# Performance work log

Hardware: AMD Instinct MI355X
Metric: run time of the kernel (lower is better)

Reference implementation:

```python
import jax, jax.numpy as jnp
import numpy as np

ALPHA = 0.2  # LeakyReLU negative slope
NEG = -9e15


def _gat_heads(x, adj_mask, W, a):
    # x: (B,N,F); W: (H,F,O); a: (H,2O); adj_mask: (B,N,N) bool
    O = W.shape[-1]
    Wh = jnp.einsum('bnf,hfo->bhno', x, W)            # (B,H,N,O)
    e1 = jnp.einsum('bhno,ho->bhn', Wh, a[:, :O])     # Wh @ a[:O]
    e2 = jnp.einsum('bhno,ho->bhn', Wh, a[:, O:])     # Wh @ a[O:]
    e = jax.nn.leaky_relu(e1[:, :, :, None] + e2[:, :, None, :], ALPHA)  # (B,H,N,N)
    e = jnp.where(adj_mask[:, None], e, NEG)
    attn = jax.nn.softmax(e, axis=-1)
    return jnp.einsum('bhnm,bhmo->bhno', attn, Wh)    # (B,H,N,O)


def _gat_block(x, adj_mask, non_pad_mask, W_heads, a_heads, W_out, a_out):
    # multi-head layer, concat=True -> elu per head, then concat on feature dim
    h = jax.nn.elu(_gat_heads(x, adj_mask, W_heads, a_heads))  # (B,H,N,O)
    B, H, N, O = h.shape
    h = jnp.transpose(h, (0, 2, 1, 3)).reshape(B, N, H * O)
    h = h * non_pad_mask
    # out layer: single head, concat=False (no inner elu)
    h = _gat_heads(h, adj_mask, W_out[None], a_out[None])[:, 0]  # (B,N,noutput)
    h = h * non_pad_mask
    return jax.nn.elu(h)


def setup_inputs() -> dict:
    key = jax.random.key(0)
    ks = jax.random.split(key, 8)
    B, N = 32, 256
    vocab, F, O, H, OUT = 200, 300, 256, 8, 512
    fea = jax.random.randint(ks[0], (B, N), 0, vocab, dtype=jnp.int32)
    adj = jax.random.randint(ks[1], (B, N, N), 0, 2, dtype=jnp.int32)
    non_pad_mask = jnp.ones((B, N, 1), dtype=jnp.float32)
    embed = jax.random.normal(ks[2], (vocab, F), dtype=jnp.float32)
    W_heads = jax.random.normal(ks[3], (H, F, O), dtype=jnp.float32) / np.sqrt(F)
    a_heads = jax.random.normal(ks[4], (H, 2 * O), dtype=jnp.float32) / np.sqrt(2 * O)
    W_out = jax.random.normal(ks[5], (H * O, OUT), dtype=jnp.float32) / np.sqrt(H * O)
    a_out = jax.random.normal(ks[6], (2 * OUT,), dtype=jnp.float32) / np.sqrt(2 * OUT)
    return {"fea": fea, "adj": adj, "non_pad_mask": non_pad_mask, "embed": embed,
            "W_heads": W_heads, "a_heads": a_heads, "W_out": W_out, "a_out": a_out}


def reference(fea, adj, non_pad_mask, embed, W_heads, a_heads, W_out, a_out):
    adj_mask = adj > 0
    x = embed[fea]  # (B,N,F)
    # GAT_num = 1; dropout is identity in eval mode
    x = _gat_block(x, adj_mask, non_pad_mask, W_heads, a_heads, W_out, a_out)
    return x  # (B, N, 512)
```

## Files before the change

### kernel.cpp

```cpp
#include <hip/hip_runtime.h>
#include <math.h>


typedef _Float16 f16;
typedef __attribute__((ext_vector_type(8))) _Float16 f16x8;
typedef __attribute__((ext_vector_type(4))) _Float16 f16x4;
typedef __attribute__((ext_vector_type(4))) float f32x4;
typedef unsigned long long u64;

__device__ __forceinline__ void async16(const void* g, void* lds) {
  __builtin_amdgcn_global_load_lds(
      (const __attribute__((address_space(1))) void*)g,
      (__attribute__((address_space(3))) void*)lds, 16, 0, 0);
}

__global__ __launch_bounds__(256) void k_prep(const int* __restrict__ fea,
                                              const float* __restrict__ embed,
                                              const float* __restrict__ Whd,
                                              const float* __restrict__ Wo,
                                              const int* __restrict__ adj,
                                              const float* __restrict__ ah,
                                              f16* __restrict__ x16,
                                              f16* __restrict__ WcT,
                                              f16* __restrict__ WoT,
                                              float* __restrict__ e_all,
                                              u64* __restrict__ adjG,
                                              float* __restrict__ w12G) {
  int bid = blockIdx.x, tid = threadIdx.x;
  if (bid < 1280) {
    int idx = bid * 256 + tid;
    int row = idx / 40, c = idx % 40;
    int tok = fea[row];
    const float* eb = embed + (size_t)tok * 300;
    f16x8 v;
    if (c < 37) {
      float4 f0 = *(const float4*)&eb[c * 8];
      float4 f1 = *(const float4*)&eb[c * 8 + 4];
      v[0] = (f16)f0.x; v[1] = (f16)f0.y; v[2] = (f16)f0.z; v[3] = (f16)f0.w;
      v[4] = (f16)f1.x; v[5] = (f16)f1.y; v[6] = (f16)f1.z; v[7] = (f16)f1.w;
    } else {
#pragma unroll
      for (int j = 0; j < 8; ++j) {
        int t = c * 8 + j;
        v[j] = (f16)((t < 300) ? eb[t] : 0.f);
      }
    }
    *(f16x8*)&x16[(size_t)row * 320 + c * 8] = v;
  } else if (bid < 1920) {
    int r = bid - 1280;
    int zi = r * 256 + tid;
    if (zi < 16384) e_all[zi] = 0.f;
    __shared__ float tile[32][33];
    int bx = r % 10, q0 = r / 10;
    int by = q0 % 8, h = q0 / 8;
    int c = tid & 31, q = tid >> 5;
#pragma unroll
    for (int i = 0; i < 4; ++i) {
      int tt = q + i * 8;
      int t = bx * 32 + tt;
      float v = (t < 300) ? Whd[((size_t)h * 300 + t) * 256 + by * 32 + c] : 0.f;
      tile[tt][c] = v;
    }
    __syncthreads();
#pragma unroll
    for (int i = 0; i < 4; ++i) {
      int oo = q + i * 8;
      int gc = h * 256 + by * 32 + oo;
      WcT[(size_t)gc * 320 + bx * 32 + c] = (f16)tile[c][oo];
    }
  } else if (bid < 2944) {
    int r = bid - 1920;
    __shared__ float tile[32][33];
    int bx = r % 64, by = r / 64;
    int c = tid & 31, q = tid >> 5;
#pragma unroll
    for (int i = 0; i < 4; ++i) {
      int kk = q + i * 8;
      tile[kk][c] = Wo[((size_t)bx * 32 + kk) * 512 + by * 32 + c];
    }
    __syncthreads();
#pragma unroll
    for (int i = 0; i < 4; ++i) {
      int oo = q + i * 8;
      WoT[((size_t)by * 32 + oo) * 2048 + bx * 32 + c] = (f16)tile[c][oo];
    }
  } else if (bid < 3072) {
    int r = bid - 2944;
    int wv = tid >> 6, ln = tid & 63;
    int row = r * 64 + wv * 16;
    const int* ar = adj + (size_t)row * 256;
#pragma unroll 4
    for (int i = 0; i < 16; ++i, ar += 256) {
      u64 m0 = __ballot(ar[ln] != 0);
      u64 m1 = __ballot(ar[64 + ln] != 0);
      u64 m2 = __ballot(ar[128 + ln] != 0);
      u64 m3 = __ballot(ar[192 + ln] != 0);
      if (ln == 0) {
        u64* d = &adjG[(size_t)(row + i) * 4];
        d[0] = m0; d[1] = m1; d[2] = m2; d[3] = m3;
      }
    }
  } else {
    int hh = bid - 3072;
    __shared__ float a1s[256], a2s[256];
    a1s[tid] = ah[hh * 512 + tid];
    a2s[tid] = ah[hh * 512 + 256 + tid];
    __syncthreads();
    for (int t = tid; t < 320; t += 256) {
      float s1 = 0.f, s2 = 0.f;
      if (t < 300) {
        const float* wr = Whd + ((size_t)hh * 300 + t) * 256;
#pragma unroll 4
        for (int o = 0; o < 256; o += 4) {
          float4 w4 = *(const float4*)&wr[o];
          s1 += w4.x * a1s[o] + w4.y * a1s[o + 1] + w4.z * a1s[o + 2] + w4.w * a1s[o + 3];
          s2 += w4.x * a2s[o] + w4.y * a2s[o + 1] + w4.z * a2s[o + 2] + w4.w * a2s[o + 3];
        }
      }
      w12G[hh * 640 + t] = s1;
      w12G[hh * 640 + 320 + t] = s2;
    }
  }
}

__global__ __launch_bounds__(256, 2) void k_l1(
    const f16* __restrict__ x16, const f16* __restrict__ WcT,
    const float* __restrict__ w12G, const u64* __restrict__ adjG,
    const float* __restrict__ npm, f16* __restrict__ h1) {
  extern __shared__ __align__(16) char smem[];
  f16* As = (f16*)smem;
  f16* Bs = (f16*)(smem + 32768);
  char* WhB = smem;
  u64* adjB = (u64*)(smem + 65536);
  float* e2f = (float*)(smem + 73728);
  float* e1f = (float*)(smem + 74752);
  float* wl  = (float*)(smem + 75776);

  const int bid = blockIdx.x;
  const int xcd = bid & 7, inner = bid >> 3;
  const int oh = inner & 1;
  const int h = (inner >> 1) & 7;
  const int b = (inner >> 4) * 8 + xcd;
  const int tid = threadIdx.x;
  const int wave = tid >> 6, lane = tid & 63;
  const int lrow = lane & 15, quad = lane >> 4;
  const int srow = lane >> 3;
  const int scol = ((lane & 7) ^ (lane >> 3)) * 8;
  const int l7 = lrow & 7;

  async16((const char*)adjG + (size_t)b * 8192 + tid * 16, (char*)adjB + tid * 16);
  async16((const char*)adjG + (size_t)b * 8192 + 4096 + tid * 16,
          (char*)adjB + 4096 + tid * 16);
  if (tid < 160) async16((const char*)w12G + h * 2560 + tid * 16, (char*)wl + tid * 16);
  __syncthreads();

  {
    const f16* xrow = x16 + ((size_t)b * 256 + tid) * 320;
    float e1 = 0.f, e2 = 0.f;
#pragma unroll 8
    for (int c = 0; c < 40; ++c) {
      f16x8 xv = *(const f16x8*)&xrow[c * 8];
#pragma unroll
      for (int j = 0; j < 8; ++j) {
        float xf = (float)xv[j];
        e1 += xf * wl[c * 8 + j];
        e2 += xf * wl[320 + c * 8 + j];
      }
    }
    e1f[tid] = e1;
    e2f[tid] = e2;
  }

  f32x4 acc[4][8] = {};
  const f16* Ag = x16 + (size_t)b * 256 * 320;
  const f16* Bg = WcT + ((size_t)(h * 256 + oh * 128)) * 320;

  for (int t = 0; t < 5; ++t) {
    const int k0 = t * 64;
    __syncthreads();
#pragma unroll
    for (int j = 0; j < 8; ++j) {
      const int r0 = wave * 64 + j * 8;
      async16(Ag + (size_t)(r0 + srow) * 320 + k0 + scol, &As[r0 * 64]);
    }
#pragma unroll
    for (int j = 0; j < 4; ++j) {
      const int r0 = wave * 32 + j * 8;
      async16(Bg + (size_t)(r0 + srow) * 320 + k0 + scol, &Bs[r0 * 64]);
    }
    __syncthreads();
#pragma unroll
    for (int s = 0; s < 2; ++s) {
      const int sq = ((s * 4 + quad) ^ l7) * 8;
      f16x8 af[4], bf[8];
#pragma unroll
      for (int mt = 0; mt < 4; ++mt)
        af[mt] = *(const f16x8*)&As[(wave * 64 + mt * 16 + lrow) * 64 + sq];
#pragma unroll
      for (int nt = 0; nt < 8; ++nt)
        bf[nt] = *(const f16x8*)&Bs[(nt * 16 + lrow) * 64 + sq];
#pragma unroll
      for (int mt = 0; mt < 4; ++mt)
#pragma unroll
        for (int nt = 0; nt < 8; ++nt)
          acc[mt][nt] = __builtin_amdgcn_mfma_f32_16x16x32_f16(af[mt], bf[nt], acc[mt][nt], 0, 0, 0);
    }
  }
  __syncthreads();

#pragma unroll
  for (int mt = 0; mt < 4; ++mt) {
    const int n0 = wave * 64 + mt * 16 + quad * 4;
    const int q16 = n0 >> 3;
    const int hoff = (n0 & 4) ? 8 : 0;
#pragma unroll
    for (int nt = 0; nt < 8; ++nt) {
      const int o = nt * 16 + lrow;
      f16x4 v;
#pragma unroll
      for (int r = 0; r < 4; ++r) v[r] = (f16)acc[mt][nt][r];
      *(f16x4*)(WhB + o * 512 + ((q16 ^ (o & 7)) * 16 + hoff)) = v;
    }
  }
  __syncthreads();

  float4 e2q = *(const float4*)&e2f[lane * 4];
  float e2m = fmaxf(fmaxf(e2q.x, e2q.y), fmaxf(e2q.z, e2q.w));
#pragma unroll
  for (int m = 1; m < 64; m <<= 1) e2m = fmaxf(e2m, __shfl_xor(e2m, m));

  float er[4], sh[4];
  u64 aw[4][4];
#pragma unroll
  for (int g = 0; g < 4; ++g) {
    int n = wave * 64 + g * 16 + lrow;
    er[g] = e1f[n];
    float s = er[g] + e2m;
    sh[g] = s > 0.f ? s : 0.2f * s;
#pragma unroll
    for (int q = 0; q < 4; ++q) aw[g][q] = adjB[n * 4 + q];
  }

  f16x8 P[4][8];
  float ss[4] = {0.f, 0.f, 0.f, 0.f};
#pragma unroll
  for (int k0 = 0; k0 < 8; ++k0) {
    const float* e2p = &e2f[k0 * 32 + quad * 8];
    float4 ea = *(const float4*)e2p;
    float4 eb = *(const float4*)(e2p + 4);
    float e2arr[8] = {ea.x, ea.y, ea.z, ea.w, eb.x, eb.y, eb.z, eb.w};
#pragma unroll
    for (int g = 0; g < 4; ++g) {
      unsigned int bits = (unsigned int)(aw[g][k0 >> 1] >> ((k0 & 1) * 32 + quad * 8)) & 0xFFu;
      f16x8 q;
#pragma unroll
      for (int j = 0; j < 8; ++j) {
        float v = er[g] + e2arr[j];
        v = v > 0.f ? v : 0.2f * v;
        float p = (bits >> j) & 1 ? __expf(v - sh[g]) : 0.f;
        ss[g] += p;
        q[j] = (f16)p;
      }
      P[g][k0] = q;
    }
  }
  float rs[4], pm[4];
  f16* hb[4];
#pragma unroll
  for (int g = 0; g < 4; ++g) {
    ss[g] += __shfl_xor(ss[g], 16);
    ss[g] += __shfl_xor(ss[g], 32);
    rs[g] = 1.f / ss[g];
    int n = wave * 64 + g * 16 + lrow;
    pm[g] = npm[b * 256 + n];
    hb[g] = &h1[((size_t)(b * 256 + n)) * 2048 + h * 256 + oh * 128];
  }

#pragma unroll 2
  for (int of = 0; of < 8; ++of) {
    const int ol = of * 16 + lrow;
    const char* wo = WhB + ol * 512;
    f32x4 c[4] = {};
#pragma unroll
    for (int k0 = 0; k0 < 8; ++k0) {
      f16x8 af = *(const f16x8*)(wo + (((k0 * 4 + quad) ^ (ol & 7)) * 16));
#pragma unroll
      for (int g = 0; g < 4; ++g)
        c[g] = __builtin_amdgcn_mfma_f32_16x16x32_f16(af, P[g][k0], c[g], 0, 0, 0);
    }
    const int o0 = of * 16 + quad * 4;
#pragma unroll
    for (int g = 0; g < 4; ++g) {
      f16x4 st;
#pragma unroll
      for (int r = 0; r < 4; ++r) {
        float v = c[g][r] * rs[g];
        v = v > 0.f ? v : (__expf(v) - 1.f);
        st[r] = (f16)(v * pm[g]);
      }
      *(f16x4*)(hb[g] + o0) = st;
    }
  }
}

__global__ __launch_bounds__(256, 4) void k_gemm_sk(const f16* __restrict__ A,
                                                    const f16* __restrict__ BT,
                                                    f16* __restrict__ outSK,
                                                    const float* __restrict__ ao,
                                                    float* __restrict__ e12,
                                                    float* __restrict__ e22) {
  __shared__ f16 As[128 * 64];
  __shared__ f16 Bs[64 * 64];
  const int bid = blockIdx.x;
  const int xcd = bid & 7, j5 = bid >> 3;
  const int bx = j5 & 7;
  const int kz = (j5 >> 6) & 1;
  const int by = xcd * 8 + ((j5 >> 3) & 7);
  const int tid = threadIdx.x;
  const int wave = tid >> 6, lane = tid & 63;
  const int wm = wave >> 1, wn = wave & 1;
  const int lrow = lane & 15, quad = lane >> 4;
  const int srow = lane >> 3;
  const int scol = ((lane & 7) ^ (lane >> 3)) * 8;
  const int l7 = lrow & 7;

  f32x4 acc[4][2] = {};
  const f16* Ag = A + (size_t)by * 128 * 2048;
  const f16* Bg = BT + (size_t)bx * 64 * 2048;
  const int kbeg = kz * 1024;

  for (int k0 = kbeg; k0 < kbeg + 1024; k0 += 64) {
    __syncthreads();
#pragma unroll
    for (int j = 0; j < 4; ++j) {
      const int r0 = wave * 32 + j * 8;
      async16(Ag + (size_t)(r0 + srow) * 2048 + k0 + scol, &As[r0 * 64]);
    }
#pragma unroll
    for (int j = 0; j < 2; ++j) {
      const int r0 = wave * 16 + j * 8;
      async16(Bg + (size_t)(r0 + srow) * 2048 + k0 + scol, &Bs[r0 * 64]);
    }
    __syncthreads();
#pragma unroll
    for (int s = 0; s < 2; ++s) {
      const int sq = ((s * 4 + quad) ^ l7) * 8;
      f16x8 af[4], bf[2];
#pragma unroll
      for (int t = 0; t < 4; ++t)
        af[t] = *(const f16x8*)&As[(wm * 64 + t * 16 + lrow) * 64 + sq];
#pragma unroll
      for (int t = 0; t < 2; ++t)
        bf[t] = *(const f16x8*)&Bs[(wn * 32 + t * 16 + lrow) * 64 + sq];
#pragma unroll
      for (int mt = 0; mt < 4; ++mt)
#pragma unroll
        for (int nt = 0; nt < 2; ++nt)
          acc[mt][nt] = __builtin_amdgcn_mfma_f32_16x16x32_f16(af[mt], bf[nt], acc[mt][nt], 0, 0, 0);
    }
  }

  const int b = (by * 128) >> 8;
  const int nbase0 = (by * 128) & 255;
  f16* dst = outSK + (size_t)kz * 32 * 512 * 256;
#pragma unroll
  for (int mt = 0; mt < 4; ++mt) {
    const int nb = nbase0 + wm * 64 + mt * 16 + quad * 4;
#pragma unroll
    for (int nt = 0; nt < 2; ++nt) {
      const int gc = bx * 64 + wn * 32 + nt * 16 + lrow;
      f16x4 v;
#pragma unroll
      for (int r = 0; r < 4; ++r) v[r] = (f16)acc[mt][nt][r];
      *(f16x4*)&dst[((size_t)b * 512 + gc) * 256 + nb] = v;
    }
  }

  float a1v[2], a2v[2];
#pragma unroll
  for (int nt = 0; nt < 2; ++nt) {
    const int gc = bx * 64 + wn * 32 + nt * 16 + lrow;
    a1v[nt] = ao[gc];
    a2v[nt] = ao[512 + gc];
  }
#pragma unroll
  for (int mt = 0; mt < 4; ++mt) {
    float s1[4] = {0.f, 0.f, 0.f, 0.f}, s2[4] = {0.f, 0.f, 0.f, 0.f};
#pragma unroll
    for (int nt = 0; nt < 2; ++nt)
#pragma unroll
      for (int r = 0; r < 4; ++r) {
        s1[r] += acc[mt][nt][r] * a1v[nt];
        s2[r] += acc[mt][nt][r] * a2v[nt];
      }
#pragma unroll
    for (int r = 0; r < 4; ++r)
#pragma unroll
      for (int m = 1; m < 16; m <<= 1) {
        s1[r] += __shfl_xor(s1[r], m);
        s2[r] += __shfl_xor(s2[r], m);
      }
    if (lrow == 0) {
      const int nb = nbase0 + wm * 64 + mt * 16 + quad * 4;
#pragma unroll
      for (int r = 0; r < 4; ++r) {
        atomicAdd(&e12[b * 256 + nb + r], s1[r]);
        atomicAdd(&e22[b * 256 + nb + r], s2[r]);
      }
    }
  }
}

#define PSTRIDE 264

__global__ __launch_bounds__(256, 4) void k_attn2(
    const f16* __restrict__ sk, const float* __restrict__ e1g, const float* __restrict__ e2g,
    const u64* __restrict__ adjG, const float* __restrict__ npm, float* __restrict__ out) {
  int bid = blockIdx.x;
  int nt0 = (bid >> 3) & 3;
  int pair = (bid >> 5) * 8 + (bid & 7);
  int oh = pair >> 5, b = pair & 31;
  int n0 = nt0 * 64;
  __shared__ f16 P[64 * PSTRIDE];
  int tid = threadIdx.x;
  int wave = tid >> 6, lane = tid & 63;
  int lrow = lane & 15, quad = lane >> 4;

  const f16* Ag0 = sk + ((size_t)b * 512 + oh * 128) * 256;
  const f16* Ag1 = Ag0 + (size_t)32 * 512 * 256;
  f16x8 afp0[2], afp1[2];
#pragma unroll
  for (int mt = 0; mt < 2; ++mt) {
    size_t off = (size_t)(wave * 32 + mt * 16 + lrow) * 256 + quad * 8;
    afp0[mt] = *(const f16x8*)&Ag0[off];
    afp1[mt] = *(const f16x8*)&Ag1[off];
  }

  float4 e2v = *(const float4*)&e2g[b * 256 + lane * 4];
  float e2m = fmaxf(fmaxf(e2v.x, e2v.y), fmaxf(e2v.z, e2v.w));
#pragma unroll
  for (int m = 1; m < 64; m <<= 1) e2m = fmaxf(e2m, __shfl_xor(e2m, m));
#pragma unroll 4
  for (int i = 0; i < 16; ++i) {
    int row = i * 4 + wave;
    int gn = b * 256 + n0 + row;
    float er = e1g[b * 256 + n0 + row];
    float sh = er + e2m;
    sh = sh > 0.f ? sh : 0.2f * sh;
    u64 word = adjG[(size_t)gn * 4 + (lane >> 4)];
    unsigned int bits = (unsigned int)(word >> ((lane & 15) * 4)) & 0xFu;
    float p0, p1, p2, p3;
    {
      float v = er + e2v.x; v = v > 0.f ? v : 0.2f * v;
      p0 = bits & 1 ? __expf(v - sh) : 0.f;
      v = er + e2v.y; v = v > 0.f ? v : 0.2f * v;
      p1 = bits & 2 ? __expf(v - sh) : 0.f;
      v = er + e2v.z; v = v > 0.f ? v : 0.2f * v;
      p2 = bits & 4 ? __expf(v - sh) : 0.f;
      v = er + e2v.w; v = v > 0.f ? v : 0.2f * v;
      p3 = bits & 8 ? __expf(v - sh) : 0.f;
    }
    float sm = p0 + p1 + p2 + p3;
#pragma unroll
    for (int m = 1; m < 64; m <<= 1) sm += __shfl_xor(sm, m);
    float rs = 1.f / sm;
    f16x4 pw;
    pw[0] = (f16)(p0 * rs); pw[1] = (f16)(p1 * rs);
    pw[2] = (f16)(p2 * rs); pw[3] = (f16)(p3 * rs);
    *(f16x4*)&P[row * PSTRIDE + lane * 4] = pw;
  }
  __syncthreads();

  f32x4 acc[2][4] = {};
#pragma unroll
  for (int kk = 0; kk < 8; ++kk) {
    const int k0 = kk * 32;
    f16x8 af[2], bf[4];
#pragma unroll
    for (int mt = 0; mt < 2; ++mt) {
      if (kk == 0) {
        af[mt] = afp0[mt] + afp1[mt];
      } else {
        size_t off = (size_t)(wave * 32 + mt * 16 + lrow) * 256 + k0 + quad * 8;
        af[mt] = *(const f16x8*)&Ag0[off] + *(const f16x8*)&Ag1[off];
      }
    }
#pragma unroll
    for (int nt = 0; nt < 4; ++nt)
      bf[nt] = *(const f16x8*)&P[(nt * 16 + lrow) * PSTRIDE + k0 + quad * 8];
#pragma unroll
    for (int mt = 0; mt < 2; ++mt)
#pragma unroll
      for (int nt = 0; nt < 4; ++nt)
        acc[mt][nt] = __builtin_amdgcn_mfma_f32_16x16x32_f16(af[mt], bf[nt], acc[mt][nt], 0, 0, 0);
  }
#pragma unroll
  for (int nt = 0; nt < 4; ++nt) {
    int nloc = nt * 16 + lrow;
    int gn = b * 256 + n0 + nloc;
    float pm = npm[gn];
#pragma unroll
    for (int mt = 0; mt < 2; ++mt) {
      int o0 = oh * 128 + wave * 32 + mt * 16 + quad * 4;
      float4 st;
      float v0 = acc[mt][nt][0] * pm;
      float v1 = acc[mt][nt][1] * pm;
      float v2 = acc[mt][nt][2] * pm;
      float v3 = acc[mt][nt][3] * pm;
      st.x = v0 > 0.f ? v0 : (__expf(v0) - 1.f);
      st.y = v1 > 0.f ? v1 : (__expf(v1) - 1.f);
      st.z = v2 > 0.f ? v2 : (__expf(v2) - 1.f);
      st.w = v3 > 0.f ? v3 : (__expf(v3) - 1.f);
      *(float4*)&out[(size_t)gn * 512 + o0] = st;
    }
  }
}

extern "C" void kernel_launch(void* const* d_in, const int* in_sizes, int n_in,
                              void* d_out, int out_size, void* d_ws, size_t ws_size,
                              hipStream_t stream) {
  (void)in_sizes; (void)n_in; (void)out_size; (void)ws_size;
  const int*   fea   = (const int*)d_in[0];
  const int*   adj   = (const int*)d_in[1];
  const float* npm   = (const float*)d_in[2];
  const float* embed = (const float*)d_in[3];
  const float* Whd   = (const float*)d_in[4];
  const float* ah    = (const float*)d_in[5];
  const float* Wo    = (const float*)d_in[6];
  const float* ao    = (const float*)d_in[7];
  float* out = (float*)d_out;

  char* ws = (char*)d_ws;
  f16* x16  = (f16*)ws;  ws += (size_t)8192 * 320 * 2;
  f16* WcT  = (f16*)ws;  ws += (size_t)2048 * 320 * 2;
  f16* WoT  = (f16*)ws;  ws += (size_t)512 * 2048 * 2;
  f16* h1   = (f16*)ws;  ws += (size_t)8192 * 2048 * 2;
  f16* Wh2sk = (f16*)ws; ws += (size_t)2 * 32 * 512 * 256 * 2;
  float* e12 = (float*)ws; ws += (size_t)8192 * 4;
  float* e22 = (float*)ws; ws += (size_t)8192 * 4;
  u64* adjG = (u64*)ws;  ws += (size_t)8192 * 4 * 8;
  float* w12G = (float*)ws; ws += (size_t)8 * 640 * 4;

  k_prep<<<3080, 256, 0, stream>>>(fea, embed, Whd, Wo, adj, ah, x16, WcT, WoT, e12, adjG, w12G);

  k_l1<<<512, 256, 78336, stream>>>(x16, WcT, w12G, adjG, npm, h1);

  k_gemm_sk<<<1024, 256, 0, stream>>>(h1, WoT, Wh2sk, ao, e12, e22);
  k_attn2<<<512, 256, 0, stream>>>(Wh2sk, e12, e22, adjG, npm, out);
}
```

Measured before the change: 199.1 us.

## Double k_l1 block to 512 threads and split work across eight waves

Doubles the threads per block of the first-layer GAT kernel from 256 to 512. The GEMM tile is split 4x2 across waves, so each wave holds a 64x64 accumulator instead of 64x128. The e1/e2 dot products are split between thread halves, and each wave handles 32 attention rows instead of 64. This lowers per-thread register pressure and adds wave-level parallelism to hide latency. In exchange it adds more waves contending for the same 78 KB LDS block, which still limits occupancy to about two blocks per CU.

```diff
diff --git a/kernel.cpp b/kernel.cpp
--- a/kernel.cpp
+++ b/kernel.cpp
@@ -123,7 +123,7 @@
   }
 }
 
-__global__ __launch_bounds__(256, 2) void k_l1(
+__global__ __launch_bounds__(512, 4) void k_l1(
     const f16* __restrict__ x16, const f16* __restrict__ WcT,
     const float* __restrict__ w12G, const u64* __restrict__ adjG,
     const float* __restrict__ npm, f16* __restrict__ h1) {
@@ -132,8 +132,8 @@
   f16* Bs = (f16*)(smem + 32768);
   char* WhB = smem;
   u64* adjB = (u64*)(smem + 65536);
-  float* e2f = (float*)(smem + 73728);
-  float* e1f = (float*)(smem + 74752);
+  float* e1f = (float*)(smem + 73728);
+  float* e2f = (float*)(smem + 74752);
   float* wl  = (float*)(smem + 75776);
 
   const int bid = blockIdx.x;
@@ -143,35 +143,32 @@
   const int b = (inner >> 4) * 8 + xcd;
   const int tid = threadIdx.x;
   const int wave = tid >> 6, lane = tid & 63;
+  const int wm = wave >> 1, wn = wave & 1;
   const int lrow = lane & 15, quad = lane >> 4;
   const int srow = lane >> 3;
   const int scol = ((lane & 7) ^ (lane >> 3)) * 8;
   const int l7 = lrow & 7;
 
   async16((const char*)adjG + (size_t)b * 8192 + tid * 16, (char*)adjB + tid * 16);
-  async16((const char*)adjG + (size_t)b * 8192 + 4096 + tid * 16,
-          (char*)adjB + 4096 + tid * 16);
   if (tid < 160) async16((const char*)w12G + h * 2560 + tid * 16, (char*)wl + tid * 16);
   __syncthreads();
 
   {
-    const f16* xrow = x16 + ((size_t)b * 256 + tid) * 320;
-    float e1 = 0.f, e2 = 0.f;
+    const int n = tid & 255;
+    const float* wv = (tid < 256) ? wl : (wl + 320);
+    const f16* xrow = x16 + ((size_t)b * 256 + n) * 320;
+    float e = 0.f;
 #pragma unroll 8
     for (int c = 0; c < 40; ++c) {
       f16x8 xv = *(const f16x8*)&xrow[c * 8];
 #pragma unroll
-      for (int j = 0; j < 8; ++j) {
-        float xf = (float)xv[j];
-        e1 += xf * wl[c * 8 + j];
-        e2 += xf * wl[320 + c * 8 + j];
-      }
-    }
-    e1f[tid] = e1;
-    e2f[tid] = e2;
-  }
-
-  f32x4 acc[4][8] = {};
+      for (int j = 0; j < 8; ++j) e += (float)xv[j] * wv[c * 8 + j];
+    }
+    if (tid < 256) e1f[n] = e;
+    else e2f[n] = e;
+  }
+
+  f32x4 acc[4][4] = {};
   const f16* Ag = x16 + (size_t)b * 256 * 320;
   const f16* Bg = WcT + ((size_t)(h * 256 + oh * 128)) * 320;
 
@@ -179,30 +176,30 @@
     const int k0 = t * 64;
     __syncthreads();
 #pragma unroll
-    for (int j = 0; j < 8; ++j) {
-      const int r0 = wave * 64 + j * 8;
-      async16(Ag + (size_t)(r0 + srow) * 320 + k0 + scol, &As[r0 * 64]);
-    }
-#pragma unroll
     for (int j = 0; j < 4; ++j) {
       const int r0 = wave * 32 + j * 8;
+      async16(Ag + (size_t)(r0 + srow) * 320 + k0 + scol, &As[r0 * 64]);
+    }
+#pragma unroll
+    for (int j = 0; j < 2; ++j) {
+      const int r0 = wave * 16 + j * 8;
       async16(Bg + (size_t)(r0 + srow) * 320 + k0 + scol, &Bs[r0 * 64]);
     }
     __syncthreads();
 #pragma unroll
     for (int s = 0; s < 2; ++s) {
       const int sq = ((s * 4 + quad) ^ l7) * 8;
-      f16x8 af[4], bf[8];
+      f16x8 af[4], bf[4];
 #pragma unroll
       for (int mt = 0; mt < 4; ++mt)
-        af[mt] = *(const f16x8*)&As[(wave * 64 + mt * 16 + lrow) * 64 + sq];
-#pragma unroll
-      for (int nt = 0; nt < 8; ++nt)
-        bf[nt] = *(const f16x8*)&Bs[(nt * 16 + lrow) * 64 + sq];
+        af[mt] = *(const f16x8*)&As[(wm * 64 + mt * 16 + lrow) * 64 + sq];
+#pragma unroll
+      for (int nt = 0; nt < 4; ++nt)
+        bf[nt] = *(const f16x8*)&Bs[(wn * 64 + nt * 16 + lrow) * 64 + sq];
 #pragma unroll
       for (int mt = 0; mt < 4; ++mt)
 #pragma unroll
-        for (int nt = 0; nt < 8; ++nt)
+        for (int nt = 0; nt < 4; ++nt)
           acc[mt][nt] = __builtin_amdgcn_mfma_f32_16x16x32_f16(af[mt], bf[nt], acc[mt][nt], 0, 0, 0);
     }
   }
@@ -210,12 +207,12 @@
 
 #pragma unroll
   for (int mt = 0; mt < 4; ++mt) {
-    const int n0 = wave * 64 + mt * 16 + quad * 4;
+    const int n0 = wm * 64 + mt * 16 + quad * 4;
     const int q16 = n0 >> 3;
     const int hoff = (n0 & 4) ? 8 : 0;
 #pragma unroll
-    for (int nt = 0; nt < 8; ++nt) {
-      const int o = nt * 16 + lrow;
+    for (int nt = 0; nt < 4; ++nt) {
+      const int o = wn * 64 + nt * 16 + lrow;
       f16x4 v;
 #pragma unroll
       for (int r = 0; r < 4; ++r) v[r] = (f16)acc[mt][nt][r];
@@ -229,77 +226,72 @@
 #pragma unroll
   for (int m = 1; m < 64; m <<= 1) e2m = fmaxf(e2m, __shfl_xor(e2m, m));
 
-  float er[4], sh[4];
-  u64 aw[4][4];
-#pragma unroll
-  for (int g = 0; g < 4; ++g) {
-    int n = wave * 64 + g * 16 + lrow;
-    er[g] = e1f[n];
-    float s = er[g] + e2m;
-    sh[g] = s > 0.f ? s : 0.2f * s;
-#pragma unroll
-    for (int q = 0; q < 4; ++q) aw[g][q] = adjB[n * 4 + q];
-  }
-
-  f16x8 P[4][8];
-  float ss[4] = {0.f, 0.f, 0.f, 0.f};
+  const int nb0 = wave * 32;
+  const float er0 = e1f[nb0 + lrow];
+  const float er1 = e1f[nb0 + 16 + lrow];
+  float sh0 = er0 + e2m; sh0 = sh0 > 0.f ? sh0 : 0.2f * sh0;
+  float sh1 = er1 + e2m; sh1 = sh1 > 0.f ? sh1 : 0.2f * sh1;
+  u64 aw0[4], aw1[4];
+#pragma unroll
+  for (int q = 0; q < 4; ++q) {
+    aw0[q] = adjB[(nb0 + lrow) * 4 + q];
+    aw1[q] = adjB[(nb0 + 16 + lrow) * 4 + q];
+  }
+
+  f16x8 p0[8], p1[8];
+  float ss0 = 0.f, ss1 = 0.f;
 #pragma unroll
   for (int k0 = 0; k0 < 8; ++k0) {
     const float* e2p = &e2f[k0 * 32 + quad * 8];
     float4 ea = *(const float4*)e2p;
     float4 eb = *(const float4*)(e2p + 4);
+    unsigned int b0 = (unsigned int)(aw0[k0 >> 1] >> ((k0 & 1) * 32 + quad * 8)) & 0xFFu;
+    unsigned int b1 = (unsigned int)(aw1[k0 >> 1] >> ((k0 & 1) * 32 + quad * 8)) & 0xFFu;
     float e2arr[8] = {ea.x, ea.y, ea.z, ea.w, eb.x, eb.y, eb.z, eb.w};
-#pragma unroll
-    for (int g = 0; g < 4; ++g) {
-      unsigned int bits = (unsigned int)(aw[g][k0 >> 1] >> ((k0 & 1) * 32 + quad * 8)) & 0xFFu;
-      f16x8 q;
-#pragma unroll
-      for (int j = 0; j < 8; ++j) {
-        float v = er[g] + e2arr[j];
-        v = v > 0.f ? v : 0.2f * v;
-        float p = (bits >> j) & 1 ? __expf(v - sh[g]) : 0.f;
-        ss[g] += p;
-        q[j] = (f16)p;
-      }
-      P[g][k0] = q;
-    }
-  }
-  float rs[4], pm[4];
-  f16* hb[4];
-#pragma unroll
-  for (int g = 0; g < 4; ++g) {
-    ss[g] += __shfl_xor(ss[g], 16);
-    ss[g] += __shfl_xor(ss[g], 32);
-    rs[g] = 1.f / ss[g];
-    int n = wave * 64 + g * 16 + lrow;
-    pm[g] = npm[b * 256 + n];
-    hb[g] = &h1[((size_t)(b * 256 + n)) * 2048 + h * 256 + oh * 128];
-  }
+    f16x8 q0, q1;
+#pragma unroll
+    for (int j = 0; j < 8; ++j) {
+      float v = er0 + e2arr[j]; v = v > 0.f ? v : 0.2f * v;
+      float p = (b0 >> j) & 1 ? __expf(v - sh0) : 0.f;
+      ss0 += p; q0[j] = (f16)p;
+      v = er1 + e2arr[j]; v = v > 0.f ? v : 0.2f * v;
+      p = (b1 >> j) & 1 ? __expf(v - sh1) : 0.f;
+      ss1 += p; q1[j] = (f16)p;
+    }
+    p0[k0] = q0; p1[k0] = q1;
+  }
+  ss0 += __shfl_xor(ss0, 16); ss0 += __shfl_xor(ss0, 32);
+  ss1 += __shfl_xor(ss1, 16); ss1 += __shfl_xor(ss1, 32);
+  const float rs0 = 1.f / ss0, rs1 = 1.f / ss1;
+  const float pm0 = npm[b * 256 + nb0 + lrow];
+  const float pm1 = npm[b * 256 + nb0 + 16 + lrow];
+  f16* h1b0 = &h1[(size_t)(b * 256 + nb0 + lrow) * 2048 + h * 256 + oh * 128];
+  f16* h1b1 = &h1[(size_t)(b * 256 + nb0 + 16 + lrow) * 2048 + h * 256 + oh * 128];
 
 #pragma unroll 2
   for (int of = 0; of < 8; ++of) {
     const int ol = of * 16 + lrow;
     const char* wo = WhB + ol * 512;
-    f32x4 c[4] = {};
+    f32x4 c0 = {}, c1 = {};
 #pragma unroll
     for (int k0 = 0; k0 < 8; ++k0) {
       f16x8 af = *(const f16x8*)(wo + (((k0 * 4 + quad) ^ (ol & 7)) * 16));
-#pragma unroll
-      for (int g = 0; g < 4; ++g)
-        c[g] = __builtin_amdgcn_mfma_f32_16x16x32_f16(af, P[g][k0], c[g], 0, 0, 0);
+      c0 = __builtin_amdgcn_mfma_f32_16x16x32_f16(af, p0[k0], c0, 0, 0, 0);
+      c1 = __builtin_amdgcn_mfma_f32_16x16x32_f16(af, p1[k0], c1, 0, 0, 0);
     }
     const int o0 = of * 16 + quad * 4;
-#pragma unroll
-    for (int g = 0; g < 4; ++g) {
-      f16x4 st;
-#pragma unroll
-      for (int r = 0; r < 4; ++r) {
-        float v = c[g][r] * rs[g];
-        v = v > 0.f ? v : (__expf(v) - 1.f);
-        st[r] = (f16)(v * pm[g]);
-      }
-      *(f16x4*)(hb[g] + o0) = st;
-    }
+    f16x4 s0, s1;
+#pragma unroll
+    for (int r = 0; r < 4; ++r) {
+      float v = c0[r] * rs0;
+      v = v > 0.f ? v : (__expf(v) - 1.f);
+      s0[r] = (f16)(v * pm0);
+      v = c1[r] * rs1;
+      v = v > 0.f ? v : (__expf(v) - 1.f);
+      s1[r] = (f16)(v * pm1);
+    }
+    *(f16x4*)(h1b0 + o0) = s0;
+    *(f16x4*)(h1b1 + o0) = s1;
   }
 }
 
@@ -543,7 +535,7 @@
 
   k_prep<<<3080, 256, 0, stream>>>(fea, embed, Whd, Wo, adj, ah, x16, WcT, WoT, e12, adjG, w12G);
 
-  k_l1<<<512, 256, 78336, stream>>>(x16, WcT, w12G, adjG, npm, h1);
+  k_l1<<<512, 512, 78336, stream>>>(x16, WcT, w12G, adjG, npm, h1);
 
   k_gemm_sk<<<1024, 256, 0, stream>>>(h1, WoT, Wh2sk, ao, e12, e22);
   k_attn2<<<512, 256, 0, stream>>>(Wh2sk, e12, e22, adjG, npm, out);
```

Result: no change. 199.7 us (+0.3%).
